# Kernel optimization log

Measured on AMD Instinct MI355X. Metric: run time of the kernel, lower is better.

Reference implementation:

```python
import jax, jax.numpy as jnp
import numpy as np

EPS = 1e-8

def _l2norm(x):
    # normalize rows, guarding against zero norm like torch cosine similarity eps
    n = jnp.sqrt(jnp.sum(x * x, axis=-1, keepdims=True))
    return x / jnp.maximum(n, EPS)

def setup_inputs() -> dict:
    key = jax.random.key(0)
    k1, k2, k3 = jax.random.split(key, 3)
    Nq, Nk, D = 4096, 4096, 1024
    return {
        "queries": jax.random.normal(k1, (Nq, D), dtype=jnp.float32),
        "keys": jax.random.normal(k2, (Nk, D), dtype=jnp.float32),
        "values": jax.random.normal(k3, (Nk, D), dtype=jnp.float32),
    }

def reference(queries, keys, values):
    # CosineSimilarityMatrix(keys, queries): [Nk, Nq] pairwise cosine sims
    attn_weights = jnp.matmul(_l2norm(keys), _l2norm(queries).T)  # [Nk, Nq]
    # weighted sum over keys for each query
    weighted = jnp.matmul(attn_weights.T, values)  # [Nq, D]
    return (weighted, attn_weights)
```

## Files before the change

### kernel.cpp

```cpp
#include <hip/hip_runtime.h>


typedef unsigned short u16;
typedef unsigned int u32;
typedef unsigned char u8;
typedef float f32x4 __attribute__((ext_vector_type(4)));
typedef int int4v __attribute__((ext_vector_type(4)));
typedef __bf16 bf16x8 __attribute__((ext_vector_type(8)));

__device__ __forceinline__ u16 f2bf(float f) {
  u32 u = __builtin_bit_cast(u32, f);
  return (u16)((u + 0x7FFFu + ((u >> 16) & 1u)) >> 16);
}

__device__ __forceinline__ void gload16(const u16* g, u16* l) {
  __builtin_amdgcn_global_load_lds((__attribute__((address_space(1))) void*)(void*)g,
                                   (__attribute__((address_space(3))) void*)(void*)l, 16, 0, 0);
}
__device__ __forceinline__ void gload16b(const u8* g, u8* l) {
  __builtin_amdgcn_global_load_lds((__attribute__((address_space(1))) void*)(void*)g,
                                   (__attribute__((address_space(3))) void*)(void*)l, 16, 0, 0);
}

#define BARRIER() __builtin_amdgcn_s_barrier()
#define WAITVM(n) asm volatile("s_waitcnt vmcnt(" #n ")" ::: "memory")
#define WAITLGKM0() do { asm volatile("s_waitcnt lgkmcnt(0)" ::: "memory"); \
                         __builtin_amdgcn_sched_barrier(0); } while (0)

__global__ __launch_bounds__(256) void norm_transv_kernel(
    const float* __restrict__ q, const float* __restrict__ k,
    u16* __restrict__ qnb, u16* __restrict__ knb,
    u8* __restrict__ qnq, u8* __restrict__ knq,
    float* __restrict__ sclQ, float* __restrict__ sclK,
    const float* __restrict__ v, u16* __restrict__ vbT) {
  int bid = blockIdx.x, t = threadIdx.x;
  if (bid < 8192) {
    const bool isQ = (bid < 4096);
    const float* src = isQ ? q : k;
    u16* dst = isQ ? qnb : knb;
    u8* dst8 = isQ ? qnq : knq;
    float* scl = isQ ? sclQ : sclK;
    int row = bid & 4095;
    const float4 val = ((const float4*)(src + (size_t)row * 1024))[t];
    float s = val.x * val.x + val.y * val.y + val.z * val.z + val.w * val.w;
    float am = fmaxf(fmaxf(fabsf(val.x), fabsf(val.y)), fmaxf(fabsf(val.z), fabsf(val.w)));
    #pragma unroll
    for (int off = 32; off > 0; off >>= 1) {
      s += __shfl_xor(s, off, 64);
      am = fmaxf(am, __shfl_xor(am, off, 64));
    }
    __shared__ float2 red[4];
    if ((t & 63) == 0) red[t >> 6] = make_float2(s, am);
    __syncthreads();
    float tot = red[0].x + red[1].x + red[2].x + red[3].x;
    float amall = fmaxf(fmaxf(red[0].y, red[1].y), fmaxf(red[2].y, red[3].y));
    float inv = 1.0f / fmaxf(sqrtf(tot), 1e-8f);
    float rm = fmaxf(amall * inv, 1e-30f);
    float iq = 127.0f / rm;
    uint2 o;
    o.x = (u32)f2bf(val.x * inv) | ((u32)f2bf(val.y * inv) << 16);
    o.y = (u32)f2bf(val.z * inv) | ((u32)f2bf(val.w * inv) << 16);
    *(uint2*)(dst + (size_t)row * 1024 + t * 4) = o;
    int c0 = (int)rintf(val.x * inv * iq);
    int c1 = (int)rintf(val.y * inv * iq);
    int c2 = (int)rintf(val.z * inv * iq);
    int c3 = (int)rintf(val.w * inv * iq);
    u32 p = (u32)(c0 & 255) | ((u32)(c1 & 255) << 8) |
            ((u32)(c2 & 255) << 16) | ((u32)(c3 & 255) << 24);
    ((u32*)(dst8 + (size_t)row * 1024))[t] = p;
    if (t == 0) scl[row] = rm * (1.0f / 127.0f);
  } else {
    __shared__ __align__(16) float lds[64 * 64];
    int tix = bid - 8192;
    int r0 = (tix >> 4) * 64, c0 = (tix & 15) * 64;
    int ch = t & 15, lr = t >> 4;
    #pragma unroll
    for (int i = 0; i < 4; ++i) {
      int r = lr + i * 16;
      float4 val = *(const float4*)&v[(size_t)(r0 + r) * 1024 + c0 + ch * 4];
      int byteoff = r * 256 + ((ch * 16) ^ (((r >> 3) & 7) << 4));
      *(float4*)((char*)lds + byteoff) = val;
    }
    __syncthreads();
    int cch = t & 7, lrow = t >> 3;
    #pragma unroll
    for (int i = 0; i < 2; ++i) {
      int oc = lrow + i * 32;
      u16 vals[8];
      #pragma unroll
      for (int j = 0; j < 8; ++j) {
        int srl = cch * 8 + j;
        int byteoff = srl * 256 + (((oc >> 2) * 16) ^ (((srl >> 3) & 7) << 4)) + (oc & 3) * 4;
        vals[j] = f2bf(*(const float*)((const char*)lds + byteoff));
      }
      uint4 o;
      o.x = (u32)vals[0] | ((u32)vals[1] << 16);
      o.y = (u32)vals[2] | ((u32)vals[3] << 16);
      o.z = (u32)vals[4] | ((u32)vals[5] << 16);
      o.w = (u32)vals[6] | ((u32)vals[7] << 16);
      *(uint4*)&vbT[(size_t)(c0 + oc) * 4096 + r0 + cch * 8] = o;
    }
  }
}

__global__ __launch_bounds__(256) void transpose_bf16_kernel(
    const u16* __restrict__ src, u16* __restrict__ dst) {
  int b = blockIdx.x;
  int r0 = (b >> 4) * 64, c0 = (b & 15) * 64;
  __shared__ __align__(16) u16 lds[64 * 64];
  int t = threadIdx.x;
  int lrow = t >> 3, cch = t & 7;
  #pragma unroll
  for (int i = 0; i < 2; ++i) {
    int sr = lrow + i * 32;
    uint4 val = *(const uint4*)&src[(size_t)(r0 + sr) * 1024 + c0 + cch * 8];
    int byteoff = sr * 128 + ((cch * 16) ^ (((sr >> 3) & 7) << 4));
    *(uint4*)((char*)lds + byteoff) = val;
  }
  __syncthreads();
  #pragma unroll
  for (int i = 0; i < 2; ++i) {
    int oc = lrow + i * 32;
    u16 vals[8];
    #pragma unroll
    for (int j = 0; j < 8; ++j) {
      int srl = cch * 8 + j;
      int byteoff = srl * 128 + ((oc * 2) ^ (cch << 4));
      vals[j] = *(const u16*)((const char*)lds + byteoff);
    }
    uint4 o;
    o.x = (u32)vals[0] | ((u32)vals[1] << 16);
    o.y = (u32)vals[2] | ((u32)vals[3] << 16);
    o.z = (u32)vals[4] | ((u32)vals[5] << 16);
    o.w = (u32)vals[6] | ((u32)vals[7] << 16);
    *(uint4*)&dst[(size_t)(c0 + oc) * 4096 + r0 + cch * 8] = o;
  }
}

template<int BM, int BN, int MW, int NW>
__global__ __launch_bounds__(256) void gemm_abt(
    const u16* __restrict__ A, const u16* __restrict__ B, float* __restrict__ Cptr,
    int k_len, int lda, int ldb, int ldc, int plane) {
  static_assert(BM == 2 * MW * 16 && BN == 2 * NW * 16, "wave grid is 2x2");
  __shared__ __align__(16) u16 ldsA[2][BM * 64];
  __shared__ __align__(16) u16 ldsB[2][BN * 64];
  const int t = threadIdx.x, l = t & 63, w = t >> 6;
  const int tileM = blockIdx.y, tileN = blockIdx.x;
  const int k_start = blockIdx.z * k_len;
  Cptr += (size_t)blockIdx.z * plane;
  const int srow = l >> 3, schunk = (l & 7) * 8;
  const u16* gA = A + (size_t)(tileM * BM) * lda + k_start + schunk;
  const u16* gB = B + (size_t)(tileN * BN) * ldb + k_start + schunk;
  const int aoff = ((w >> 1) * MW * 16 + (l & 15)) * 64 + (l >> 4) * 8;
  const int boff = ((w & 1) * NW * 16 + (l & 15)) * 64 + (l >> 4) * 8;

  f32x4 acc[MW][NW];
  #pragma unroll
  for (int m = 0; m < MW; ++m)
    #pragma unroll
    for (int n = 0; n < NW; ++n) acc[m][n] = (f32x4){0.f, 0.f, 0.f, 0.f};

  auto stage = [&](int buf, int kof) {
    #pragma unroll
    for (int j = 0; j < BM / 32; ++j) {
      const int r = w * (BM / 4) + j * 8;
      gload16(gA + (size_t)(r + srow) * lda + kof, &ldsA[buf][r * 64]);
    }
    #pragma unroll
    for (int j = 0; j < BN / 32; ++j) {
      const int r = w * (BN / 4) + j * 8;
      gload16(gB + (size_t)(r + srow) * ldb + kof, &ldsB[buf][r * 64]);
    }
  };

  bf16x8 av0[MW], bv0[NW], av1[MW], bv1[NW];
  const int nt = k_len >> 6;
  stage(0, 0);
  __syncthreads();
  #pragma unroll
  for (int m = 0; m < MW; ++m) av0[m] = *(const bf16x8*)&ldsA[0][aoff + m * 16 * 64];
  #pragma unroll
  for (int n = 0; n < NW; ++n) bv0[n] = *(const bf16x8*)&ldsB[0][boff + n * 16 * 64];

  for (int i = 0; i < nt; ++i) {
    const int cur = i & 1;
    if (i + 1 < nt) stage(cur ^ 1, (i + 1) * 64);
    #pragma unroll
    for (int m = 0; m < MW; ++m) av1[m] = *(const bf16x8*)&ldsA[cur][aoff + m * 16 * 64 + 32];
    #pragma unroll
    for (int n = 0; n < NW; ++n) bv1[n] = *(const bf16x8*)&ldsB[cur][boff + n * 16 * 64 + 32];
    #pragma unroll
    for (int m = 0; m < MW; ++m)
      #pragma unroll
      for (int n = 0; n < NW; ++n)
        acc[m][n] = __builtin_amdgcn_mfma_f32_16x16x32_bf16(av0[m], bv0[n], acc[m][n], 0, 0, 0);
    #pragma unroll
    for (int m = 0; m < MW; ++m)
      #pragma unroll
      for (int n = 0; n < NW; ++n)
        acc[m][n] = __builtin_amdgcn_mfma_f32_16x16x32_bf16(av1[m], bv1[n], acc[m][n], 0, 0, 0);
    __syncthreads();
    if (i + 1 < nt) {
      const int nxt = cur ^ 1;
      #pragma unroll
      for (int m = 0; m < MW; ++m) av0[m] = *(const bf16x8*)&ldsA[nxt][aoff + m * 16 * 64];
      #pragma unroll
      for (int n = 0; n < NW; ++n) bv0[n] = *(const bf16x8*)&ldsB[nxt][boff + n * 16 * 64];
    }
  }

  const int orow = tileM * BM + (w >> 1) * MW * 16 + (l >> 4) * 4;
  const int ocol = tileN * BN + (w & 1) * NW * 16 + (l & 15);
  #pragma unroll
  for (int m = 0; m < MW; ++m)
    #pragma unroll
    for (int n = 0; n < NW; ++n)
      #pragma unroll
      for (int r = 0; r < 4; ++r)
        Cptr[(size_t)(orow + m * 16 + r) * ldc + (ocol + n * 16)] = acc[m][n][r];
}

__global__ __launch_bounds__(512, 2) void gemm256_i8(
    const u8* __restrict__ A8, const u8* __restrict__ B8, float* __restrict__ C,
    const float* __restrict__ P, u16* __restrict__ ctred,
    const float* __restrict__ sclK, const float* __restrict__ sclQ, int ntn) {
  __shared__ __align__(16) u8 lds8[131072];
  const int tid = threadIdx.x, l = tid & 63, w = tid >> 6;
  const int wm = w >> 2, wn = w & 3;
  const int nwg = gridDim.x * gridDim.y;
  const int bid = blockIdx.y * gridDim.x + blockIdx.x;
  const int swz = (bid & 7) * (nwg >> 3) + (bid >> 3);
  const int tileM = swz / ntn, tileN = swz % ntn;

  const int r0 = w * 32 + (l >> 2);
  const int s0 = ((l & 3) ^ ((l >> 3) & 3)) * 16;
  const int offA = r0 * 1024 + s0;
  const u8* gA8 = A8 + (size_t)tileM * 256 * 1024;
  const u8* gB8 = B8 + (size_t)tileN * 256 * 1024;

#define STGA8(kof, bb) do { \
    gload16b(gA8 + (kof) + offA,          lds8 + (bb) + w * 2048); \
    gload16b(gA8 + (kof) + offA + 16384,  lds8 + (bb) + w * 2048 + 1024); } while (0)
#define STGB8(kof, bb) do { \
    gload16b(gB8 + (kof) + offA,          lds8 + (bb) + 16384 + w * 2048); \
    gload16b(gB8 + (kof) + offA + 16384,  lds8 + (bb) + 16384 + w * 2048 + 1024); } while (0)

  STGA8(0, 0);        STGB8(0, 0);
  STGA8(64, 32768);   STGB8(64, 32768);
  STGA8(128, 65536);  STGB8(128, 65536);
  STGA8(192, 98304);  STGB8(192, 98304);
  {
    const int base = bid * 4096 + tid * 8;
    f32x4 sa = *(const f32x4*)&P[base];
    f32x4 sb = *(const f32x4*)&P[base + 4];
    #pragma unroll
    for (int p = 1; p < 4; ++p) {
      sa += *(const f32x4*)&P[(size_t)p * 1048576 + base];
      sb += *(const f32x4*)&P[(size_t)p * 1048576 + base + 4];
    }
    uint4 o;
    o.x = (u32)f2bf(sa[0]) | ((u32)f2bf(sa[1]) << 16);
    o.y = (u32)f2bf(sa[2]) | ((u32)f2bf(sa[3]) << 16);
    o.z = (u32)f2bf(sb[0]) | ((u32)f2bf(sb[1]) << 16);
    o.w = (u32)f2bf(sb[2]) | ((u32)f2bf(sb[3]) << 16);
    *(uint4*)&ctred[base] = o;
  }
  WAITVM(0);
  BARRIER();

  const int scol = ((l >> 4) ^ ((l >> 1) & 3)) * 16;
  const int afragB = (wm * 128 + (l & 15)) * 64 + scol;
  const int bfragB = (wn * 64 + (l & 15)) * 64 + scol;

  int4v acc[8][4];
  #pragma unroll
  for (int m = 0; m < 8; ++m)
    #pragma unroll
    for (int n = 0; n < 4; ++n) acc[m][n] = (int4v){0, 0, 0, 0};

  int4v A0[4], A1[4], B0[4];
  #pragma unroll
  for (int m = 0; m < 4; ++m) A0[m] = *(const int4v*)&lds8[afragB + m * 1024];
  #pragma unroll
  for (int n = 0; n < 4; ++n) B0[n] = *(const int4v*)&lds8[16384 + bfragB + n * 1024];

  const int NT = 16;
  for (int t = 0; t < NT; ++t) {
    const int bb = (t & 3) * 32768;
    const int koff = t * 64;
    #pragma unroll
    for (int m = 0; m < 4; ++m) A1[m] = *(const int4v*)&lds8[bb + afragB + (m + 4) * 1024];
    BARRIER();
    WAITLGKM0();
    __builtin_amdgcn_s_setprio(1);
    #pragma unroll
    for (int m = 0; m < 4; ++m)
      #pragma unroll
      for (int n = 0; n < 4; ++n)
        acc[m][n] = __builtin_amdgcn_mfma_i32_16x16x64_i8(A0[m], B0[n], acc[m][n], 0, 0, 0);
    __builtin_amdgcn_s_setprio(0);
    BARRIER();
    if (t + 4 < NT) { STGA8(koff + 256, bb); STGB8(koff + 256, bb); }
    __builtin_amdgcn_s_setprio(1);
    #pragma unroll
    for (int m = 0; m < 4; ++m)
      #pragma unroll
      for (int n = 0; n < 4; ++n)
        acc[m + 4][n] = __builtin_amdgcn_mfma_i32_16x16x64_i8(A1[m], B0[n], acc[m + 4][n], 0, 0, 0);
    __builtin_amdgcn_s_setprio(0);
    if (t + 4 < NT)      { WAITVM(12); }
    else if (t + 3 < NT) { WAITVM(8); }
    else if (t + 2 < NT) { WAITVM(4); }
    else if (t + 1 < NT) { WAITVM(0); }
    BARRIER();
    if (t + 1 < NT) {
      const int nb = ((t + 1) & 3) * 32768;
      #pragma unroll
      for (int m = 0; m < 4; ++m) A0[m] = *(const int4v*)&lds8[nb + afragB + m * 1024];
      #pragma unroll
      for (int n = 0; n < 4; ++n) B0[n] = *(const int4v*)&lds8[nb + 16384 + bfragB + n * 1024];
    }
  }

  const int orow = tileM * 256 + wm * 128 + (l >> 4) * 4;
  const int ocol = tileN * 256 + wn * 64 + (l & 15);
  float sq[4];
  #pragma unroll
  for (int n = 0; n < 4; ++n) sq[n] = sclQ[ocol + n * 16];
  #pragma unroll
  for (int m = 0; m < 8; ++m) {
    const float4 sk4 = *(const float4*)&sclK[orow + m * 16];
    #pragma unroll
    for (int n = 0; n < 4; ++n)
      #pragma unroll
      for (int r = 0; r < 4; ++r)
        C[(size_t)(orow + m * 16 + r) * 4096 + (ocol + n * 16)] =
            (float)acc[m][n][r] * ((const float*)&sk4)[r] * sq[n];
  }
#undef STGA8
#undef STGB8
}

extern "C" void kernel_launch(void* const* d_in, const int* in_sizes, int n_in,
                              void* d_out, int out_size, void* d_ws, size_t ws_size,
                              hipStream_t stream) {
  const float* q = (const float*)d_in[0];
  const float* k = (const float*)d_in[1];
  const float* v = (const float*)d_in[2];
  float* out = (float*)d_out;
  float* weighted = out;
  float* attn = out + 4194304;

  char* ws = (char*)d_ws;
  u16* qnb = (u16*)(ws);
  u16* knb = (u16*)(ws + (8u << 20));
  u16* knT = (u16*)(ws + (16u << 20));
  u16* vbT = (u16*)(ws + (24u << 20));
  u16* ct  = (u16*)(ws + (32u << 20));
  u8*  qnq = (u8*)(ws + (34u << 20));
  u8*  knq = (u8*)(ws + (38u << 20));
  float* sclQ = (float*)(ws + (42u << 20));
  float* sclK = (float*)(ws + (42u << 20) + 65536);

  norm_transv_kernel<<<9216, 256, 0, stream>>>(q, k, qnb, knb, qnq, knq, sclQ, sclK, v, vbT);
  transpose_bf16_kernel<<<1024, 256, 0, stream>>>(knb, knT);
  gemm_abt<128, 64, 4, 2><<<dim3(16, 8, 4), 256, 0, stream>>>(
      vbT, knT, weighted, 1024, 4096, 4096, 1024, 1048576);
  gemm256_i8<<<dim3(16, 16), 512, 0, stream>>>(
      knq, qnq, attn, weighted, ct, sclK, sclQ, 16);
  gemm_abt<128, 64, 4, 2><<<dim3(16, 32, 1), 256, 0, stream>>>(
      qnb, ct, weighted, 1024, 1024, 1024, 1024, 0);
}
```

Measured before the change: 88.22 us.

## Shrink int8 GEMM tile to 256x128 with triple-buffered LDS pipeline

The int8 attention-weight GEMM tile goes from 256x256 to 256x128, doubling the grid to 512 workgroups. LDS buffering drops from four stages of 32KB to three stages of 24KB, so two workgroups can share a CU. The K-loop is reordered: the prefetch is issued at the top and barriers are removed from the middle of the loop. The split-K partial reduction per block is halved to match the new grid. Better occupancy and load balance across CUs come at the cost of less operand reuse per tile and a shallower prefetch depth.

```diff
diff --git a/kernel.cpp b/kernel.cpp
--- a/kernel.cpp
+++ b/kernel.cpp
@@ -220,11 +220,11 @@
         Cptr[(size_t)(orow + m * 16 + r) * ldc + (ocol + n * 16)] = acc[m][n][r];
 }
 
-__global__ __launch_bounds__(512, 2) void gemm256_i8(
+__global__ __launch_bounds__(512, 4) void gemm256_i8(
     const u8* __restrict__ A8, const u8* __restrict__ B8, float* __restrict__ C,
     const float* __restrict__ P, u16* __restrict__ ctred,
     const float* __restrict__ sclK, const float* __restrict__ sclQ, int ntn) {
-  __shared__ __align__(16) u8 lds8[131072];
+  __shared__ __align__(16) u8 lds8[73728];
   const int tid = threadIdx.x, l = tid & 63, w = tid >> 6;
   const int wm = w >> 2, wn = w & 3;
   const int nwg = gridDim.x * gridDim.y;
@@ -232,113 +232,97 @@
   const int swz = (bid & 7) * (nwg >> 3) + (bid >> 3);
   const int tileM = swz / ntn, tileN = swz % ntn;
 
-  const int r0 = w * 32 + (l >> 2);
-  const int s0 = ((l & 3) ^ ((l >> 3) & 3)) * 16;
-  const int offA = r0 * 1024 + s0;
+  const int offA = (tid >> 2) * 1024 + (((tid & 3) ^ ((tid >> 3) & 3)) << 4);
   const u8* gA8 = A8 + (size_t)tileM * 256 * 1024;
-  const u8* gB8 = B8 + (size_t)tileN * 256 * 1024;
-
-#define STGA8(kof, bb) do { \
-    gload16b(gA8 + (kof) + offA,          lds8 + (bb) + w * 2048); \
-    gload16b(gA8 + (kof) + offA + 16384,  lds8 + (bb) + w * 2048 + 1024); } while (0)
-#define STGB8(kof, bb) do { \
-    gload16b(gB8 + (kof) + offA,          lds8 + (bb) + 16384 + w * 2048); \
-    gload16b(gB8 + (kof) + offA + 16384,  lds8 + (bb) + 16384 + w * 2048 + 1024); } while (0)
-
-  STGA8(0, 0);        STGB8(0, 0);
-  STGA8(64, 32768);   STGB8(64, 32768);
-  STGA8(128, 65536);  STGB8(128, 65536);
-  STGA8(192, 98304);  STGB8(192, 98304);
+  const u8* gB8 = B8 + (size_t)tileN * 128 * 1024;
+
+#define STG(kof, bb) do { \
+    gload16b(gA8 + (kof) + offA,          lds8 + (bb) + w * 1024); \
+    gload16b(gA8 + (kof) + offA + 131072, lds8 + (bb) + 8192 + w * 1024); \
+    gload16b(gB8 + (kof) + offA,          lds8 + (bb) + 16384 + w * 1024); } while (0)
+
+  STG(0, 0);
+  STG(64, 24576);
   {
-    const int base = bid * 4096 + tid * 8;
-    f32x4 sa = *(const f32x4*)&P[base];
-    f32x4 sb = *(const f32x4*)&P[base + 4];
-    #pragma unroll
-    for (int p = 1; p < 4; ++p) {
-      sa += *(const f32x4*)&P[(size_t)p * 1048576 + base];
-      sb += *(const f32x4*)&P[(size_t)p * 1048576 + base + 4];
-    }
-    uint4 o;
-    o.x = (u32)f2bf(sa[0]) | ((u32)f2bf(sa[1]) << 16);
-    o.y = (u32)f2bf(sa[2]) | ((u32)f2bf(sa[3]) << 16);
-    o.z = (u32)f2bf(sb[0]) | ((u32)f2bf(sb[1]) << 16);
-    o.w = (u32)f2bf(sb[2]) | ((u32)f2bf(sb[3]) << 16);
-    *(uint4*)&ctred[base] = o;
+    const int base = bid * 2048 + tid * 4;
+    f32x4 s = *(const f32x4*)&P[base];
+    #pragma unroll
+    for (int p = 1; p < 4; ++p) s += *(const f32x4*)&P[(size_t)p * 1048576 + base];
+    uint2 o;
+    o.x = (u32)f2bf(s[0]) | ((u32)f2bf(s[1]) << 16);
+    o.y = (u32)f2bf(s[2]) | ((u32)f2bf(s[3]) << 16);
+    *(uint2*)&ctred[base] = o;
   }
   WAITVM(0);
   BARRIER();
 
-  const int scol = ((l >> 4) ^ ((l >> 1) & 3)) * 16;
+  const int scol = (((l >> 4) ^ ((l >> 1) & 3)) << 4);
   const int afragB = (wm * 128 + (l & 15)) * 64 + scol;
-  const int bfragB = (wn * 64 + (l & 15)) * 64 + scol;
-
-  int4v acc[8][4];
+  const int bfragB = 16384 + (wn * 32 + (l & 15)) * 64 + scol;
+
+  int4v acc[8][2];
   #pragma unroll
   for (int m = 0; m < 8; ++m)
     #pragma unroll
-    for (int n = 0; n < 4; ++n) acc[m][n] = (int4v){0, 0, 0, 0};
-
-  int4v A0[4], A1[4], B0[4];
+    for (int n = 0; n < 2; ++n) acc[m][n] = (int4v){0, 0, 0, 0};
+
+  int4v A0[4], A1[4], B0[2];
   #pragma unroll
   for (int m = 0; m < 4; ++m) A0[m] = *(const int4v*)&lds8[afragB + m * 1024];
   #pragma unroll
-  for (int n = 0; n < 4; ++n) B0[n] = *(const int4v*)&lds8[16384 + bfragB + n * 1024];
+  for (int n = 0; n < 2; ++n) B0[n] = *(const int4v*)&lds8[bfragB + n * 1024];
 
   const int NT = 16;
   for (int t = 0; t < NT; ++t) {
-    const int bb = (t & 3) * 32768;
-    const int koff = t * 64;
-    #pragma unroll
-    for (int m = 0; m < 4; ++m) A1[m] = *(const int4v*)&lds8[bb + afragB + (m + 4) * 1024];
-    BARRIER();
+    const int bb = (t % 3) * 24576;
+    if (t + 2 < NT) STG((t + 2) * 64, ((t + 2) % 3) * 24576);
     WAITLGKM0();
     __builtin_amdgcn_s_setprio(1);
     #pragma unroll
     for (int m = 0; m < 4; ++m)
       #pragma unroll
-      for (int n = 0; n < 4; ++n)
+      for (int n = 0; n < 2; ++n)
         acc[m][n] = __builtin_amdgcn_mfma_i32_16x16x64_i8(A0[m], B0[n], acc[m][n], 0, 0, 0);
     __builtin_amdgcn_s_setprio(0);
-    BARRIER();
-    if (t + 4 < NT) { STGA8(koff + 256, bb); STGB8(koff + 256, bb); }
+    #pragma unroll
+    for (int m = 0; m < 4; ++m) A1[m] = *(const int4v*)&lds8[bb + afragB + (m + 4) * 1024];
+    WAITLGKM0();
     __builtin_amdgcn_s_setprio(1);
     #pragma unroll
     for (int m = 0; m < 4; ++m)
       #pragma unroll
-      for (int n = 0; n < 4; ++n)
+      for (int n = 0; n < 2; ++n)
         acc[m + 4][n] = __builtin_amdgcn_mfma_i32_16x16x64_i8(A1[m], B0[n], acc[m + 4][n], 0, 0, 0);
     __builtin_amdgcn_s_setprio(0);
-    if (t + 4 < NT)      { WAITVM(12); }
-    else if (t + 3 < NT) { WAITVM(8); }
-    else if (t + 2 < NT) { WAITVM(4); }
-    else if (t + 1 < NT) { WAITVM(0); }
+    if (t + 1 < NT) {
+      if (t + 2 < NT) { WAITVM(3); } else { WAITVM(0); }
+    }
     BARRIER();
     if (t + 1 < NT) {
-      const int nb = ((t + 1) & 3) * 32768;
+      const int nb = ((t + 1) % 3) * 24576;
       #pragma unroll
       for (int m = 0; m < 4; ++m) A0[m] = *(const int4v*)&lds8[nb + afragB + m * 1024];
       #pragma unroll
-      for (int n = 0; n < 4; ++n) B0[n] = *(const int4v*)&lds8[nb + 16384 + bfragB + n * 1024];
+      for (int n = 0; n < 2; ++n) B0[n] = *(const int4v*)&lds8[nb + bfragB + n * 1024];
     }
   }
 
   const int orow = tileM * 256 + wm * 128 + (l >> 4) * 4;
-  const int ocol = tileN * 256 + wn * 64 + (l & 15);
-  float sq[4];
-  #pragma unroll
-  for (int n = 0; n < 4; ++n) sq[n] = sclQ[ocol + n * 16];
+  const int ocol = tileN * 128 + wn * 32 + (l & 15);
+  float sq[2];
+  #pragma unroll
+  for (int n = 0; n < 2; ++n) sq[n] = sclQ[ocol + n * 16];
   #pragma unroll
   for (int m = 0; m < 8; ++m) {
     const float4 sk4 = *(const float4*)&sclK[orow + m * 16];
     #pragma unroll
-    for (int n = 0; n < 4; ++n)
+    for (int n = 0; n < 2; ++n)
       #pragma unroll
       for (int r = 0; r < 4; ++r)
         C[(size_t)(orow + m * 16 + r) * 4096 + (ocol + n * 16)] =
             (float)acc[m][n][r] * ((const float*)&sk4)[r] * sq[n];
   }
-#undef STGA8
-#undef STGB8
+#undef STG
 }
 
 extern "C" void kernel_launch(void* const* d_in, const int* in_sizes, int n_in,
@@ -366,8 +350,8 @@
   transpose_bf16_kernel<<<1024, 256, 0, stream>>>(knb, knT);
   gemm_abt<128, 64, 4, 2><<<dim3(16, 8, 4), 256, 0, stream>>>(
       vbT, knT, weighted, 1024, 4096, 4096, 1024, 1048576);
-  gemm256_i8<<<dim3(16, 16), 512, 0, stream>>>(
-      knq, qnq, attn, weighted, ct, sclK, sclQ, 16);
+  gemm256_i8<<<dim3(32, 16), 512, 0, stream>>>(
+      knq, qnq, attn, weighted, ct, sclK, sclQ, 32);
   gemm_abt<128, 64, 4, 2><<<dim3(16, 32, 1), 256, 0, stream>>>(
       qnb, ct, weighted, 1024, 1024, 1024, 1024, 0);
 }
```

Result: no change. 88.59 us (+0.4%).

## Triple-buffer LDS in bf16 gemm_abt with vmcnt-based partial waits

Applied to the files above, without the earlier changes.

Changes the bf16 A·B^T GEMM from double to triple buffering in LDS, prefetching two k-tiles ahead. It replaces the full __syncthreads with a partial vmcnt wait (WAITVM(6)) plus a raw barrier, so one stage's global loads can stay in flight across the barrier. The aim is to hide global-load latency better. In exchange it uses 1.5x the LDS, which may lower occupancy, and hardcodes the assumption of 6 loads per thread per stage.

```diff
diff --git a/kernel.cpp b/kernel.cpp
--- a/kernel.cpp
+++ b/kernel.cpp
@@ -142,8 +142,9 @@
     const u16* __restrict__ A, const u16* __restrict__ B, float* __restrict__ Cptr,
     int k_len, int lda, int ldb, int ldc, int plane) {
   static_assert(BM == 2 * MW * 16 && BN == 2 * NW * 16, "wave grid is 2x2");
-  __shared__ __align__(16) u16 ldsA[2][BM * 64];
-  __shared__ __align__(16) u16 ldsB[2][BN * 64];
+  static_assert(BM / 32 + BN / 32 == 6, "WAITVM(6) literal assumes 6 loads/thread/stage");
+  constexpr int TILE = (BM + BN) * 64;
+  __shared__ __align__(16) u16 lds[3 * TILE];
   const int t = threadIdx.x, l = t & 63, w = t >> 6;
   const int tileM = blockIdx.y, tileN = blockIdx.x;
   const int k_start = blockIdx.z * k_len;
@@ -152,7 +153,7 @@
   const u16* gA = A + (size_t)(tileM * BM) * lda + k_start + schunk;
   const u16* gB = B + (size_t)(tileN * BN) * ldb + k_start + schunk;
   const int aoff = ((w >> 1) * MW * 16 + (l & 15)) * 64 + (l >> 4) * 8;
-  const int boff = ((w & 1) * NW * 16 + (l & 15)) * 64 + (l >> 4) * 8;
+  const int boff = BM * 64 + ((w & 1) * NW * 16 + (l & 15)) * 64 + (l >> 4) * 8;
 
   f32x4 acc[MW][NW];
   #pragma unroll
@@ -161,34 +162,37 @@
     for (int n = 0; n < NW; ++n) acc[m][n] = (f32x4){0.f, 0.f, 0.f, 0.f};
 
   auto stage = [&](int buf, int kof) {
+    u16* bb = lds + buf * TILE;
     #pragma unroll
     for (int j = 0; j < BM / 32; ++j) {
       const int r = w * (BM / 4) + j * 8;
-      gload16(gA + (size_t)(r + srow) * lda + kof, &ldsA[buf][r * 64]);
+      gload16(gA + (size_t)(r + srow) * lda + kof, bb + r * 64);
     }
     #pragma unroll
     for (int j = 0; j < BN / 32; ++j) {
       const int r = w * (BN / 4) + j * 8;
-      gload16(gB + (size_t)(r + srow) * ldb + kof, &ldsB[buf][r * 64]);
+      gload16(gB + (size_t)(r + srow) * ldb + kof, bb + BM * 64 + r * 64);
     }
   };
 
   bf16x8 av0[MW], bv0[NW], av1[MW], bv1[NW];
   const int nt = k_len >> 6;
   stage(0, 0);
-  __syncthreads();
-  #pragma unroll
-  for (int m = 0; m < MW; ++m) av0[m] = *(const bf16x8*)&ldsA[0][aoff + m * 16 * 64];
-  #pragma unroll
-  for (int n = 0; n < NW; ++n) bv0[n] = *(const bf16x8*)&ldsB[0][boff + n * 16 * 64];
+  if (nt > 1) { stage(1, 64); WAITVM(6); }
+  else        { WAITVM(0); }
+  BARRIER();
+  #pragma unroll
+  for (int m = 0; m < MW; ++m) av0[m] = *(const bf16x8*)&lds[aoff + m * 16 * 64];
+  #pragma unroll
+  for (int n = 0; n < NW; ++n) bv0[n] = *(const bf16x8*)&lds[boff + n * 16 * 64];
 
   for (int i = 0; i < nt; ++i) {
-    const int cur = i & 1;
-    if (i + 1 < nt) stage(cur ^ 1, (i + 1) * 64);
-    #pragma unroll
-    for (int m = 0; m < MW; ++m) av1[m] = *(const bf16x8*)&ldsA[cur][aoff + m * 16 * 64 + 32];
-    #pragma unroll
-    for (int n = 0; n < NW; ++n) bv1[n] = *(const bf16x8*)&ldsB[cur][boff + n * 16 * 64 + 32];
+    const u16* bb = lds + (i % 3) * TILE;
+    if (i + 2 < nt) stage((i + 2) % 3, (i + 2) * 64);
+    #pragma unroll
+    for (int m = 0; m < MW; ++m) av1[m] = *(const bf16x8*)&bb[aoff + m * 16 * 64 + 32];
+    #pragma unroll
+    for (int n = 0; n < NW; ++n) bv1[n] = *(const bf16x8*)&bb[boff + n * 16 * 64 + 32];
     #pragma unroll
     for (int m = 0; m < MW; ++m)
       #pragma unroll
@@ -199,13 +203,16 @@
       #pragma unroll
       for (int n = 0; n < NW; ++n)
         acc[m][n] = __builtin_amdgcn_mfma_f32_16x16x32_bf16(av1[m], bv1[n], acc[m][n], 0, 0, 0);
-    __syncthreads();
     if (i + 1 < nt) {
-      const int nxt = cur ^ 1;
-      #pragma unroll
-      for (int m = 0; m < MW; ++m) av0[m] = *(const bf16x8*)&ldsA[nxt][aoff + m * 16 * 64];
-      #pragma unroll
-      for (int n = 0; n < NW; ++n) bv0[n] = *(const bf16x8*)&ldsB[nxt][boff + n * 16 * 64];
+      if (i + 2 < nt) { WAITVM(6); } else { WAITVM(0); }
+    }
+    BARRIER();
+    if (i + 1 < nt) {
+      const u16* nb = lds + ((i + 1) % 3) * TILE;
+      #pragma unroll
+      for (int m = 0; m < MW; ++m) av0[m] = *(const bf16x8*)&nb[aoff + m * 16 * 64];
+      #pragma unroll
+      for (int n = 0; n < NW; ++n) bv0[n] = *(const bf16x8*)&nb[boff + n * 16 * 64];
     }
   }
 
```

Result: no change. 88.28 us (+0.1%).
